# Performance work log

Measured on AMD Instinct MI355X. Metric: run time of the kernel, lower is better.

Reference implementation:

```python
import jax, jax.numpy as jnp
import numpy as np

B, N, D_MODEL, HEADS, DFF, M = 4, 4096, 1024, 16, 4096, 256
DH = D_MODEL // HEADS  # 64
EPS_K = 1e-4
LN_EPS = 1e-5


def setup_inputs() -> dict:
    key = jax.random.key(0)
    ks = jax.random.split(key, 12)
    s = 0.02
    return {
        "video": jax.random.normal(ks[0], (B, N, D_MODEL), jnp.float32),
        "Wq": jax.random.normal(ks[1], (D_MODEL, D_MODEL), jnp.float32) * s,
        "bq": jnp.zeros((D_MODEL,), jnp.float32),
        "Wk": jax.random.normal(ks[2], (D_MODEL, D_MODEL), jnp.float32) * s,
        "bk": jnp.zeros((D_MODEL,), jnp.float32),
        "Wv": jax.random.normal(ks[3], (D_MODEL, D_MODEL), jnp.float32) * s,
        "bv": jnp.zeros((D_MODEL,), jnp.float32),
        "Wo": jax.random.normal(ks[4], (D_MODEL, D_MODEL), jnp.float32) * s,
        "bo": jnp.zeros((D_MODEL,), jnp.float32),
        "proj": jax.random.normal(ks[5], (M, DH), jnp.float32),  # random-feature matrix (buffer)
        "W1": jax.random.normal(ks[6], (DFF, D_MODEL), jnp.float32) * s,
        "b1": jnp.zeros((DFF,), jnp.float32),
        "W2": jax.random.normal(ks[7], (D_MODEL, DFF), jnp.float32) * s,
        "b2": jnp.zeros((D_MODEL,), jnp.float32),
        "g2": jnp.ones((D_MODEL,), jnp.float32),
        "be2": jnp.zeros((D_MODEL,), jnp.float32),
        "g3": jnp.ones((D_MODEL,), jnp.float32),
        "be3": jnp.zeros((D_MODEL,), jnp.float32),
    }


def softmax_kernel(x, proj, is_query):
    # FAVOR+ positive softmax random features (Performer).
    # x: [b,h,n,dh], proj: [m,dh]
    norm = x.shape[-1] ** -0.25  # data normalizer 1/d^{1/4}
    ratio = proj.shape[0] ** -0.5
    xp = jnp.einsum("bhnd,md->bhnm", x * norm, proj)
    diag = jnp.sum(jnp.square(x), axis=-1, keepdims=True) * 0.5 * (norm * norm)
    if is_query:
        stab = jnp.max(xp, axis=-1, keepdims=True)
    else:
        stab = jnp.max(xp, axis=(-1, -2), keepdims=True)
    return ratio * (jnp.exp(xp - diag - stab) + EPS_K)


def layer_norm(x, g, b):
    mu = jnp.mean(x, axis=-1, keepdims=True)
    var = jnp.mean(jnp.square(x - mu), axis=-1, keepdims=True)
    return (x - mu) * jax.lax.rsqrt(var + LN_EPS) * g + b


def reference(video, Wq, bq, Wk, bk, Wv, bv, Wo, bo, proj,
              W1, b1, W2, b2, g2, be2, g3, be3):
    b, n, d = video.shape
    split = lambda t: t.reshape(b, n, HEADS, DH).transpose(0, 2, 1, 3)  # [b,h,n,dh]
    q = split(video @ Wq.T + bq)
    k = split(video @ Wk.T + bk)
    v = split(video @ Wv.T + bv)

    qp = softmax_kernel(q, proj, is_query=True)   # [b,h,n,m]
    kp = softmax_kernel(k, proj, is_query=False)  # [b,h,n,m]

    # Non-causal linear attention: O(n*m*dh) instead of O(n^2)
    k_sum = jnp.sum(kp, axis=2)                              # [b,h,m]
    denom = jnp.einsum("bhnm,bhm->bhn", qp, k_sum)           # [b,h,n]
    ctx = jnp.einsum("bhnm,bhnd->bhmd", kp, v)               # [b,h,m,dh]
    out = jnp.einsum("bhnm,bhmd->bhnd", qp, ctx) / denom[..., None]

    attn = out.transpose(0, 2, 1, 3).reshape(b, n, d) @ Wo.T + bo
    x = layer_norm(video + attn, g2, be2)  # dropout is identity in eval
    ff = jax.nn.relu(x @ W1.T + b1) @ W2.T + b2
    return layer_norm(x + ff, g3, be3)
```

## Files before the change

kernel.cpp:

```cpp
#include <hip/hip_runtime.h>
#include <hip/hip_bf16.h>

#define N_TOK   4096
#define DMODEL  1024
#define NHEADS  16
#define DH      64
#define MFEAT   256
#define DFF     4096
#define BATCH   4
#define ROWS    (BATCH * N_TOK)

#define NORMF      0.35355339059327373f
#define HALF_NORM2 0.0625f
#define RATIO      0.0625f
#define EPSK       1e-4f
#define LNEPS      1e-5f

typedef unsigned short ushort_t;
using bfrag = __attribute__((ext_vector_type(8))) short;
using facc  = __attribute__((ext_vector_type(4))) float;
using ush8  = __attribute__((ext_vector_type(8))) unsigned short;

__device__ __forceinline__ float b2f(ushort_t u) {
    return __bfloat162float(__builtin_bit_cast(__hip_bfloat16, u));
}
__device__ __forceinline__ ushort_t f2b(float f) {
    return __builtin_bit_cast(ushort_t, __float2bfloat16(f));
}
__device__ __forceinline__ void stC(float* p, float v) { *p = v; }
__device__ __forceinline__ void stC(ushort_t* p, float v) { *p = f2b(v); }

__device__ __forceinline__ void gload_lds16(const void* g, void* l) {
    __builtin_amdgcn_global_load_lds(
        (const __attribute__((address_space(1))) unsigned int*)g,
        (__attribute__((address_space(3))) unsigned int*)l, 16, 0, 0);
}

__device__ __forceinline__ unsigned fkey(float f) {
    unsigned u = __float_as_uint(f);
    return (u & 0x80000000u) ? ~u : (u | 0x80000000u);
}
__device__ __forceinline__ float fdec(unsigned k) {
    return (k & 0x80000000u) ? __uint_as_float(k ^ 0x80000000u) : __uint_as_float(~k);
}

__global__ __launch_bounds__(256) void cvt_bf16(const float* __restrict__ s,
                                                ushort_t* __restrict__ d, int n4) {
    int i = blockIdx.x * 256 + threadIdx.x;
    if (i >= n4) return;
    float4 v = ((const float4*)s)[i];
    ((ushort4*)d)[i] = make_ushort4(f2b(v.x), f2b(v.y), f2b(v.z), f2b(v.w));
}

template <int FJ, typename OT>
__global__ __launch_bounds__(256) void gemm_mfma(
    const ushort_t* __restrict__ A, const ushort_t* __restrict__ W,
    const float* __restrict__ bias, OT* __restrict__ C,
    int Nout, int K, int relu)
{
    constexpr int BN = FJ * 32;
    __shared__ short As[2][128 * 32];
    __shared__ short Ws[2][BN * 32];
    const int t = threadIdx.x;
    const unsigned nwg = gridDim.x * gridDim.y;
    const unsigned flat = blockIdx.y * gridDim.x + blockIdx.x;
    const unsigned cpx = nwg >> 3;
    const unsigned wg = (flat & 7) * cpx + (flat >> 3);
    const int m0 = (int)(wg / gridDim.x) * 128, n0 = (int)(wg % gridDim.x) * BN;
    const int lane = t & 63, wave = t >> 6;
    const int wr = (wave >> 1) * 64, wc = (wave & 1) * (FJ * 16);
    const int lm = lane & 15, kq = (lane >> 4) * 8;
    facc acc[4][FJ];
#pragma unroll
    for (int i = 0; i < 4; ++i)
#pragma unroll
        for (int j = 0; j < FJ; ++j) acc[i][j] = (facc){0.f, 0.f, 0.f, 0.f};

    auto stage = [&](int b, int k0) {
#pragma unroll
        for (int it = 0; it < 2; ++it) {
            int ch = t + it * 256;
            gload_lds16(A + (size_t)(m0 + (ch >> 2)) * K + k0 + (ch & 3) * 8, &As[b][ch * 8]);
        }
#pragma unroll
        for (int it = 0; it < BN / 64; ++it) {
            int ch = t + it * 256;
            gload_lds16(W + (size_t)(n0 + (ch >> 2)) * K + k0 + (ch & 3) * 8, &Ws[b][ch * 8]);
        }
    };

    stage(0, 0);
    __syncthreads();
    int buf = 0;
    for (int k0 = 0; k0 < K; k0 += 32) {
        if (k0 + 32 < K) stage(buf ^ 1, k0 + 32);
        bfrag af[4], bf[FJ];
#pragma unroll
        for (int i = 0; i < 4; ++i) af[i] = *(bfrag*)&As[buf][(wr + i * 16 + lm) * 32 + kq];
#pragma unroll
        for (int j = 0; j < FJ; ++j) bf[j] = *(bfrag*)&Ws[buf][(wc + j * 16 + lm) * 32 + kq];
#pragma unroll
        for (int i = 0; i < 4; ++i)
#pragma unroll
            for (int j = 0; j < FJ; ++j)
                acc[i][j] = __builtin_amdgcn_mfma_f32_16x16x32_bf16(af[i], bf[j], acc[i][j], 0, 0, 0);
        __syncthreads();
        buf ^= 1;
    }
    const int rq = (lane >> 4) * 4;
#pragma unroll
    for (int i = 0; i < 4; ++i)
#pragma unroll
        for (int j = 0; j < FJ; ++j) {
            int col = n0 + wc + j * 16 + lm;
            float bc = bias[col];
#pragma unroll
            for (int r = 0; r < 4; ++r) {
                int row = m0 + wr + i * 16 + rq + r;
                float v = acc[i][j][r] + bc;
                if (relu) v = fmaxf(v, 0.f);
                stC(C + (size_t)row * Nout + col, v);
            }
        }
}

__global__ __launch_bounds__(256) void gemm_kv(
    const ushort_t* __restrict__ A,
    const ushort_t* __restrict__ WK, const ushort_t* __restrict__ WV,
    const float* __restrict__ bK, const float* __restrict__ bV,
    ushort_t* __restrict__ CK, ushort_t* __restrict__ CV)
{
    __shared__ short As[2][128 * 32];
    __shared__ short Ws[2][128 * 32];
    const int t = threadIdx.x;
    const unsigned nwg = gridDim.x * gridDim.y;
    const unsigned flat = blockIdx.y * gridDim.x + blockIdx.x;
    const unsigned cpx = nwg >> 3;
    const unsigned wg = (flat & 7) * cpx + (flat >> 3);
    const int m0 = (int)(wg / gridDim.x) * 128;
    const int nt = (int)(wg % gridDim.x);
    const ushort_t* W = (nt < 8) ? WK : WV;
    const float* bias = (nt < 8) ? bK : bV;
    ushort_t* C = (nt < 8) ? CK : CV;
    const int n0 = (nt & 7) * 128;
    const int lane = t & 63, wave = t >> 6;
    const int wr = (wave >> 1) * 64, wc = (wave & 1) * 64;
    const int lm = lane & 15, kq = (lane >> 4) * 8;
    facc acc[4][4];
#pragma unroll
    for (int i = 0; i < 4; ++i)
#pragma unroll
        for (int j = 0; j < 4; ++j) acc[i][j] = (facc){0.f, 0.f, 0.f, 0.f};

    auto stage = [&](int b, int k0) {
#pragma unroll
        for (int it = 0; it < 2; ++it) {
            int ch = t + it * 256;
            gload_lds16(A + (size_t)(m0 + (ch >> 2)) * DMODEL + k0 + (ch & 3) * 8, &As[b][ch * 8]);
            gload_lds16(W + (size_t)(n0 + (ch >> 2)) * DMODEL + k0 + (ch & 3) * 8, &Ws[b][ch * 8]);
        }
    };

    stage(0, 0);
    __syncthreads();
    int buf = 0;
    for (int k0 = 0; k0 < DMODEL; k0 += 32) {
        if (k0 + 32 < DMODEL) stage(buf ^ 1, k0 + 32);
        bfrag af[4], bf[4];
#pragma unroll
        for (int i = 0; i < 4; ++i) af[i] = *(bfrag*)&As[buf][(wr + i * 16 + lm) * 32 + kq];
#pragma unroll
        for (int j = 0; j < 4; ++j) bf[j] = *(bfrag*)&Ws[buf][(wc + j * 16 + lm) * 32 + kq];
#pragma unroll
        for (int i = 0; i < 4; ++i)
#pragma unroll
            for (int j = 0; j < 4; ++j)
                acc[i][j] = __builtin_amdgcn_mfma_f32_16x16x32_bf16(af[i], bf[j], acc[i][j], 0, 0, 0);
        __syncthreads();
        buf ^= 1;
    }
    const int rq = (lane >> 4) * 4;
#pragma unroll
    for (int i = 0; i < 4; ++i)
#pragma unroll
        for (int j = 0; j < 4; ++j) {
            int col = n0 + wc + j * 16 + lm;
            float bc = bias[col];
#pragma unroll
            for (int r = 0; r < 4; ++r) {
                int row = m0 + wr + i * 16 + rq + r;
                C[(size_t)row * DMODEL + col] = f2b(acc[i][j][r] + bc);
            }
        }
}

__global__ __launch_bounds__(256) void vt_kernel(
    const ushort_t* __restrict__ V, ushort_t* __restrict__ VT)
{
    __shared__ ushort_t tile[64][68];
    const int t = threadIdx.x;
    const int n0 = blockIdx.x * 64, h = blockIdx.y;
#pragma unroll
    for (int i = 0; i < 4; ++i) {
        int idx = t + i * 256;
        int nl = idx >> 4, d4 = (idx & 15) * 4;
        ushort4 v = *(const ushort4*)(V + (size_t)(n0 + nl) * DMODEL + h * DH + d4);
        tile[nl][d4 + 0] = v.x; tile[nl][d4 + 1] = v.y;
        tile[nl][d4 + 2] = v.z; tile[nl][d4 + 3] = v.w;
    }
    __syncthreads();
#pragma unroll
    for (int i = 0; i < 4; ++i) {
        int idx = t + i * 256;
        int d = idx >> 4, n4 = (idx & 15) * 4;
        ushort4 o = make_ushort4(tile[n4][d], tile[n4 + 1][d], tile[n4 + 2][d], tile[n4 + 3][d]);
        *(ushort4*)(VT + (size_t)h * DH * N_TOK + (size_t)d * N_TOK + n0 + n4) = o;
    }
}

__global__ __launch_bounds__(256) void diagk_kernel(
    const ushort_t* __restrict__ Kb, float* __restrict__ diagK)
{
    const int lane = threadIdx.x & 63, wave = threadIdx.x >> 6;
    const int n = blockIdx.x * 4 + wave;
    const ushort_t* kr = Kb + (size_t)n * DMODEL + lane * 16;
    ush8 a = *(const ush8*)kr;
    ush8 b = *(const ush8*)(kr + 8);
    float s = 0.f;
#pragma unroll
    for (int e = 0; e < 8; ++e) { float x = b2f(a[e]); s += x * x; }
#pragma unroll
    for (int e = 0; e < 8; ++e) { float x = b2f(b[e]); s += x * x; }
    s += __shfl_xor(s, 1);
    s += __shfl_xor(s, 2);
    if ((lane & 3) == 0) diagK[(size_t)(lane >> 2) * N_TOK + n] = s;
}

__global__ __launch_bounds__(256) void xk_kernel(
    const ushort_t* __restrict__ projBF,
    const ushort_t* __restrict__ Kb,
    const float* __restrict__ diagK,
    unsigned* __restrict__ kmax16,
    ushort_t* __restrict__ KP,
    int mode)
{
    __shared__ short As[2][128 * 32];
    __shared__ short Ws[2][128 * 32];
    const int t = threadIdx.x;
    const int m0 = blockIdx.x * 128, n0 = blockIdx.y * 128, h = blockIdx.z;
    const ushort_t* Kh = Kb + h * DH;
    const int lane = t & 63, wave = t >> 6;
    const int wr = (wave >> 1) * 64, wc = (wave & 1) * 64;
    const int lm = lane & 15, kq = (lane >> 4) * 8;
    facc acc[4][4];
#pragma unroll
    for (int i = 0; i < 4; ++i)
#pragma unroll
        for (int j = 0; j < 4; ++j) acc[i][j] = (facc){0.f, 0.f, 0.f, 0.f};

    auto stage = [&](int b, int k0) {
#pragma unroll
        for (int it = 0; it < 2; ++it) {
            int ch = t + it * 256;
            gload_lds16(projBF + (size_t)(m0 + (ch >> 2)) * DH + k0 + (ch & 3) * 8, &As[b][ch * 8]);
            gload_lds16(Kh + (size_t)(n0 + (ch >> 2)) * DMODEL + k0 + (ch & 3) * 8, &Ws[b][ch * 8]);
        }
    };

    stage(0, 0);
    __syncthreads();
    int buf = 0;
    for (int k0 = 0; k0 < DH; k0 += 32) {
        if (k0 + 32 < DH) stage(buf ^ 1, k0 + 32);
        bfrag af[4], bf[4];
#pragma unroll
        for (int i = 0; i < 4; ++i) af[i] = *(bfrag*)&As[buf][(wr + i * 16 + lm) * 32 + kq];
#pragma unroll
        for (int j = 0; j < 4; ++j) bf[j] = *(bfrag*)&Ws[buf][(wc + j * 16 + lm) * 32 + kq];
#pragma unroll
        for (int i = 0; i < 4; ++i)
#pragma unroll
            for (int j = 0; j < 4; ++j)
                acc[i][j] = __builtin_amdgcn_mfma_f32_16x16x32_bf16(af[i], bf[j], acc[i][j], 0, 0, 0);
        __syncthreads();
        buf ^= 1;
    }
    const int rq = (lane >> 4) * 4;
    if (mode == 0) {
        float mx = -1e30f;
#pragma unroll
        for (int i = 0; i < 4; ++i)
#pragma unroll
            for (int j = 0; j < 4; ++j)
#pragma unroll
                for (int r = 0; r < 4; ++r) mx = fmaxf(mx, acc[i][j][r]);
        mx *= NORMF;
#pragma unroll
        for (int o = 32; o >= 1; o >>= 1) mx = fmaxf(mx, __shfl_xor(mx, o));
        if (lane == 0) atomicMax(kmax16 + h, fkey(mx));
    } else {
        const float stab = fdec(kmax16[h]);
        ushort_t* kb = KP + (size_t)h * MFEAT * N_TOK;
#pragma unroll
        for (int j = 0; j < 4; ++j) {
            int n = n0 + wc + j * 16 + lm;
            float dg = HALF_NORM2 * diagK[(size_t)h * N_TOK + n] + stab;
#pragma unroll
            for (int i = 0; i < 4; ++i)
#pragma unroll
                for (int r = 0; r < 4; ++r) {
                    int m = m0 + wr + i * 16 + rq + r;
                    float x = NORMF * acc[i][j][r];
                    kb[(size_t)m * N_TOK + n] = f2b(RATIO * (expf(x - dg) + EPSK));
                }
        }
    }
}

__global__ __launch_bounds__(256) void ksum_kernel(
    const ushort_t* __restrict__ KP, float* __restrict__ ksum)
{
    const int lane = threadIdx.x & 63, wave = threadIdx.x >> 6;
    const int row = blockIdx.x * 4 + wave;
    const ushort_t* kr = KP + (size_t)row * N_TOK;
    float s = 0.f;
#pragma unroll
    for (int it = 0; it < 8; ++it) {
        ush8 v = *(const ush8*)(kr + it * 512 + lane * 8);
#pragma unroll
        for (int e = 0; e < 8; ++e) s += b2f(v[e]);
    }
#pragma unroll
    for (int o = 32; o >= 1; o >>= 1) s += __shfl_xor(s, o);
    if (lane == 0) ksum[row] = s;
}

__global__ __launch_bounds__(256) void ctx_mfma(
    const ushort_t* __restrict__ KP, const ushort_t* __restrict__ VT,
    float* __restrict__ ctxp)
{
    __shared__ short As[2][128 * 32];
    __shared__ short Vs[2][64 * 32];
    const int t = threadIdx.x;
    const int z = blockIdx.x, mh = blockIdx.y, h = blockIdx.z;
    const ushort_t* A = KP + (size_t)h * MFEAT * N_TOK + (size_t)mh * 128 * N_TOK;
    const ushort_t* W = VT + (size_t)h * DH * N_TOK;
    const int lane = t & 63, wave = t >> 6;
    const int wr = (wave >> 1) * 64, wc = (wave & 1) * 32;
    const int lm = lane & 15, kq = (lane >> 4) * 8;
    facc acc[4][2];
#pragma unroll
    for (int i = 0; i < 4; ++i)
#pragma unroll
        for (int j = 0; j < 2; ++j) acc[i][j] = (facc){0.f, 0.f, 0.f, 0.f};

    auto stage = [&](int b, int k0) {
#pragma unroll
        for (int it = 0; it < 2; ++it) {
            int ch = t + it * 256;
            gload_lds16(A + (size_t)(ch >> 2) * N_TOK + k0 + (ch & 3) * 8, &As[b][ch * 8]);
        }
        gload_lds16(W + (size_t)(t >> 2) * N_TOK + k0 + (t & 3) * 8, &Vs[b][t * 8]);
    };

    const int kbeg = z * 512, kend = kbeg + 512;
    stage(0, kbeg);
    __syncthreads();
    int buf = 0;
    for (int k0 = kbeg; k0 < kend; k0 += 32) {
        if (k0 + 32 < kend) stage(buf ^ 1, k0 + 32);
        bfrag af[4], bf[2];
#pragma unroll
        for (int i = 0; i < 4; ++i) af[i] = *(bfrag*)&As[buf][(wr + i * 16 + lm) * 32 + kq];
#pragma unroll
        for (int j = 0; j < 2; ++j) bf[j] = *(bfrag*)&Vs[buf][(wc + j * 16 + lm) * 32 + kq];
#pragma unroll
        for (int i = 0; i < 4; ++i)
#pragma unroll
            for (int j = 0; j < 2; ++j)
                acc[i][j] = __builtin_amdgcn_mfma_f32_16x16x32_bf16(af[i], bf[j], acc[i][j], 0, 0, 0);
        __syncthreads();
        buf ^= 1;
    }
    const int rq = (lane >> 4) * 4;
    float* cb = ctxp + ((size_t)(z * NHEADS + h) * MFEAT + mh * 128) * DH;
#pragma unroll
    for (int i = 0; i < 4; ++i)
#pragma unroll
        for (int j = 0; j < 2; ++j)
#pragma unroll
            for (int r = 0; r < 4; ++r) {
                int m = wr + i * 16 + rq + r;
                int d = wc + j * 16 + lm;
                cb[(size_t)m * DH + d] = acc[i][j][r];
            }
}

__global__ __launch_bounds__(256) void ctx_transpose(
    const float* __restrict__ ctxp, ushort_t* __restrict__ ctxT)
{
    __shared__ float tile[64][65];
    const int h = blockIdx.x >> 2, mb = blockIdx.x & 3, t = threadIdx.x;
#pragma unroll
    for (int i = 0; i < 16; ++i) {
        int idx = t + i * 256;
        int ml = idx >> 6, d = idx & 63;
        int m = mb * 64 + ml;
        float s = 0.f;
#pragma unroll
        for (int z = 0; z < 8; ++z)
            s += ctxp[((size_t)(z * NHEADS + h) * MFEAT + m) * DH + d];
        tile[ml][d] = s;
    }
    __syncthreads();
    ushort_t* ob = ctxT + (size_t)h * DH * MFEAT;
#pragma unroll
    for (int i = 0; i < 16; ++i) {
        int idx = t + i * 256;
        int d = idx >> 6, ml = idx & 63;
        ob[(size_t)d * MFEAT + mb * 64 + ml] = f2b(tile[ml][d]);
    }
}

__global__ __launch_bounds__(256) void xp_gemm(
    const float* __restrict__ Q, const ushort_t* __restrict__ projBF,
    ushort_t* __restrict__ XP)
{
    __shared__ short As[128][40];
    __shared__ short Ws[128][40];
    const int t = threadIdx.x;
    const int m0 = blockIdx.x * 128, n0v = blockIdx.y * 128, h = blockIdx.z;
    const float* Qb = Q + h * DH;
    const int lane = t & 63, wave = t >> 6;
    const int wr = (wave >> 1) * 64, wc = (wave & 1) * 64;
    const int lm = lane & 15, kq = (lane >> 4) * 8;
    facc acc[4][4];
#pragma unroll
    for (int i = 0; i < 4; ++i)
#pragma unroll
        for (int j = 0; j < 4; ++j) acc[i][j] = (facc){0.f, 0.f, 0.f, 0.f};

    for (int k0 = 0; k0 < 64; k0 += 32) {
#pragma unroll
        for (int it = 0; it < 4; ++it) {
            int ch = t + it * 256;
            int row = ch >> 3, c4 = (ch & 7) * 4;
            float4 v = *(const float4*)(Qb + (size_t)(n0v + row) * DMODEL + k0 + c4);
            As[row][c4 + 0] = (short)f2b(v.x);
            As[row][c4 + 1] = (short)f2b(v.y);
            As[row][c4 + 2] = (short)f2b(v.z);
            As[row][c4 + 3] = (short)f2b(v.w);
        }
#pragma unroll
        for (int it = 0; it < 2; ++it) {
            int ch = t + it * 256;
            int row = ch >> 2, c8 = (ch & 3) * 8;
            *(uint4*)&Ws[row][c8] = *(const uint4*)(projBF + (size_t)(m0 + row) * DH + k0 + c8);
        }
        __syncthreads();
        bfrag af[4], bf[4];
#pragma unroll
        for (int i = 0; i < 4; ++i) af[i] = *(bfrag*)&As[wr + i * 16 + lm][kq];
#pragma unroll
        for (int j = 0; j < 4; ++j) bf[j] = *(bfrag*)&Ws[wc + j * 16 + lm][kq];
#pragma unroll
        for (int i = 0; i < 4; ++i)
#pragma unroll
            for (int j = 0; j < 4; ++j)
                acc[i][j] = __builtin_amdgcn_mfma_f32_16x16x32_bf16(af[i], bf[j], acc[i][j], 0, 0, 0);
        __syncthreads();
    }
    const int rq = (lane >> 4) * 4;
    ushort_t* xb = XP + (size_t)h * N_TOK * MFEAT;
#pragma unroll
    for (int i = 0; i < 4; ++i)
#pragma unroll
        for (int j = 0; j < 4; ++j) {
            int col = m0 + wc + j * 16 + lm;
#pragma unroll
            for (int r = 0; r < 4; ++r) {
                int row = n0v + wr + i * 16 + rq + r;
                xb[(size_t)row * MFEAT + col] = f2b(NORMF * acc[i][j][r]);
            }
        }
}

__global__ __launch_bounds__(256) void qp_kernel(
    ushort_t* __restrict__ XP, const float* __restrict__ Q,
    const float* __restrict__ ksum, float* __restrict__ denom)
{
    const int lane = threadIdx.x & 63, wave = threadIdx.x >> 6;
    const int row0 = (blockIdx.x * 4 + wave) * 8;
    for (int rr = 0; rr < 8; ++rr) {
        const int row = row0 + rr;
        const int h = row >> 12, n = row & 4095;
        ushort_t* xr = XP + (size_t)row * MFEAT + lane * 4;
        ushort4 xv = *(ushort4*)xr;
        float x0 = b2f(xv.x), x1 = b2f(xv.y), x2 = b2f(xv.z), x3 = b2f(xv.w);
        float qv = Q[(size_t)n * DMODEL + h * DH + lane];
        float ss = qv * qv;
#pragma unroll
        for (int o = 32; o >= 1; o >>= 1) ss += __shfl_xor(ss, o);
        float mx = fmaxf(fmaxf(x0, x1), fmaxf(x2, x3));
#pragma unroll
        for (int o = 32; o >= 1; o >>= 1) mx = fmaxf(mx, __shfl_xor(mx, o));
        const float sh = HALF_NORM2 * ss + mx;
        float p0 = RATIO * (expf(x0 - sh) + EPSK);
        float p1 = RATIO * (expf(x1 - sh) + EPSK);
        float p2 = RATIO * (expf(x2 - sh) + EPSK);
        float p3 = RATIO * (expf(x3 - sh) + EPSK);
        ushort4 pv = make_ushort4(f2b(p0), f2b(p1), f2b(p2), f2b(p3));
        *(ushort4*)xr = pv;
        float4 ks4 = *(const float4*)(ksum + h * MFEAT + lane * 4);
        float dn = b2f(pv.x) * ks4.x + b2f(pv.y) * ks4.y + b2f(pv.z) * ks4.z + b2f(pv.w) * ks4.w;
#pragma unroll
        for (int o = 32; o >= 1; o >>= 1) dn += __shfl_xor(dn, o);
        if (lane == 0) denom[row] = dn;
    }
}

__global__ __launch_bounds__(256) void out_gemm(
    const ushort_t* __restrict__ XP, const ushort_t* __restrict__ ctxT,
    const float* __restrict__ denom, ushort_t* __restrict__ OUT)
{
    __shared__ short As[2][128 * 32];
    __shared__ short Ws[2][64 * 32];
    const int t = threadIdx.x;
    const int n0 = blockIdx.x * 128, h = blockIdx.y;
    const ushort_t* A = XP + (size_t)h * N_TOK * MFEAT;
    const ushort_t* W = ctxT + (size_t)h * DH * MFEAT;
    const float* dnb = denom + (size_t)h * N_TOK;
    ushort_t* ob = OUT + h * DH;
    const int lane = t & 63, wave = t >> 6;
    const int wr = (wave >> 1) * 64, wc = (wave & 1) * 32;
    const int lm = lane & 15, kq = (lane >> 4) * 8;
    facc acc[4][2];
#pragma unroll
    for (int i = 0; i < 4; ++i)
#pragma unroll
        for (int j = 0; j < 2; ++j) acc[i][j] = (facc){0.f, 0.f, 0.f, 0.f};

    auto stage = [&](int b, int k0) {
#pragma unroll
        for (int it = 0; it < 2; ++it) {
            int ch = t + it * 256;
            gload_lds16(A + (size_t)(n0 + (ch >> 2)) * MFEAT + k0 + (ch & 3) * 8, &As[b][ch * 8]);
        }
        gload_lds16(W + (size_t)(t >> 2) * MFEAT + k0 + (t & 3) * 8, &Ws[b][t * 8]);
    };

    stage(0, 0);
    __syncthreads();
    int buf = 0;
    for (int k0 = 0; k0 < MFEAT; k0 += 32) {
        if (k0 + 32 < MFEAT) stage(buf ^ 1, k0 + 32);
        bfrag af[4], bf[2];
#pragma unroll
        for (int i = 0; i < 4; ++i) af[i] = *(bfrag*)&As[buf][(wr + i * 16 + lm) * 32 + kq];
#pragma unroll
        for (int j = 0; j < 2; ++j) bf[j] = *(bfrag*)&Ws[buf][(wc + j * 16 + lm) * 32 + kq];
#pragma unroll
        for (int i = 0; i < 4; ++i)
#pragma unroll
            for (int j = 0; j < 2; ++j)
                acc[i][j] = __builtin_amdgcn_mfma_f32_16x16x32_bf16(af[i], bf[j], acc[i][j], 0, 0, 0);
        __syncthreads();
        buf ^= 1;
    }
    const int rq = (lane >> 4) * 4;
#pragma unroll
    for (int i = 0; i < 4; ++i)
#pragma unroll
        for (int r = 0; r < 4; ++r) {
            int row = n0 + wr + i * 16 + rq + r;
            float inv = 1.f / dnb[row];
#pragma unroll
            for (int j = 0; j < 2; ++j) {
                int col = wc + j * 16 + lm;
                ob[(size_t)row * DMODEL + col] = f2b(acc[i][j][r] * inv);
            }
        }
}

__global__ __launch_bounds__(256) void ln_kernel(
    const float* __restrict__ A, const void* __restrict__ Badd, int badd_bf16,
    const float* __restrict__ g, const float* __restrict__ bb,
    float* __restrict__ out, ushort_t* __restrict__ out_bf)
{
    __shared__ float red[8];
    const int row = blockIdx.x, t = threadIdx.x;
    const int lane = t & 63, wave = t >> 6;
    float4 av = ((const float4*)(A + (size_t)row * DMODEL))[t];
    float a0, a1, a2, a3;
    if (badd_bf16) {
        ushort4 bv4 = ((const ushort4*)Badd)[(size_t)row * (DMODEL / 4) + t];
        a0 = b2f(bv4.x); a1 = b2f(bv4.y); a2 = b2f(bv4.z); a3 = b2f(bv4.w);
    } else {
        float4 bf4 = ((const float4*)Badd)[(size_t)row * (DMODEL / 4) + t];
        a0 = bf4.x; a1 = bf4.y; a2 = bf4.z; a3 = bf4.w;
    }
    float v0 = av.x + a0, v1 = av.y + a1, v2 = av.z + a2, v3 = av.w + a3;
    float s = v0 + v1 + v2 + v3;
#pragma unroll
    for (int o = 32; o >= 1; o >>= 1) s += __shfl_xor(s, o);
    if (lane == 0) red[wave] = s;
    __syncthreads();
    float mu = (red[0] + red[1] + red[2] + red[3]) * (1.f / DMODEL);
    float d0 = v0 - mu, d1 = v1 - mu, d2 = v2 - mu, d3 = v3 - mu;
    float sq = d0 * d0 + d1 * d1 + d2 * d2 + d3 * d3;
#pragma unroll
    for (int o = 32; o >= 1; o >>= 1) sq += __shfl_xor(sq, o);
    if (lane == 0) red[4 + wave] = sq;
    __syncthreads();
    float rstd = rsqrtf((red[4] + red[5] + red[6] + red[7]) * (1.f / DMODEL) + LNEPS);
    float4 gv = ((const float4*)g)[t];
    float4 bv = ((const float4*)bb)[t];
    float o0 = d0 * rstd * gv.x + bv.x;
    float o1 = d1 * rstd * gv.y + bv.y;
    float o2 = d2 * rstd * gv.z + bv.z;
    float o3 = d3 * rstd * gv.w + bv.w;
    ((float4*)(out + (size_t)row * DMODEL))[t] = make_float4(o0, o1, o2, o3);
    if (out_bf)
        ((ushort4*)(out_bf + (size_t)row * DMODEL))[t] =
            make_ushort4(f2b(o0), f2b(o1), f2b(o2), f2b(o3));
}

extern "C" void kernel_launch(void* const* d_in, const int* in_sizes, int n_in,
                              void* d_out, int out_size, void* d_ws, size_t ws_size,
                              hipStream_t stream)
{
    const float* video = (const float*)d_in[0];
    const float* Wq = (const float*)d_in[1];
    const float* bq = (const float*)d_in[2];
    const float* Wk = (const float*)d_in[3];
    const float* bk = (const float*)d_in[4];
    const float* Wv = (const float*)d_in[5];
    const float* bv = (const float*)d_in[6];
    const float* Wo = (const float*)d_in[7];
    const float* bo = (const float*)d_in[8];
    const float* proj = (const float*)d_in[9];
    const float* W1 = (const float*)d_in[10];
    const float* b1 = (const float*)d_in[11];
    const float* W2 = (const float*)d_in[12];
    const float* b2 = (const float*)d_in[13];
    const float* g2 = (const float*)d_in[14];
    const float* be2 = (const float*)d_in[15];
    const float* g3 = (const float*)d_in[16];
    const float* be3 = (const float*)d_in[17];

    char* ws = (char*)d_ws;
    const size_t MB = 1048576ull;
    ushort_t* videoBF = (ushort_t*)(ws + 0);
    ushort_t* Kb   = (ushort_t*)(ws + 32 * MB);
    ushort_t* XBFb = (ushort_t*)(ws + 32 * MB);
    ushort_t* Vb   = (ushort_t*)(ws + 40 * MB);
    ushort_t* Fb   = (ushort_t*)(ws + 40 * MB);
    ushort_t* VTb  = (ushort_t*)(ws + 48 * MB);
    ushort_t* Yb   = (ushort_t*)(ws + 48 * MB);
    ushort_t* KP   = (ushort_t*)(ws + 56 * MB);
    ushort_t* Hb   = (ushort_t*)(ws + 56 * MB);
    ushort_t* ctxTb = (ushort_t*)(ws + 93847552ull + MB);
    char* smalls = ws + 91 * MB + 393216ull;
    float*    diagK  = (float*)(smalls);
    float*    ksum   = (float*)(smalls + 262144);
    float*    denomB = (float*)(smalls + 278528);
    unsigned* kmax16 = (unsigned*)(smalls + 540672);
    ushort_t* projBF = (ushort_t*)(smalls + 541184);
    float*    ctxp  = (float*)(ws + 92 * MB);
    ushort_t* OUTb = (ushort_t*)(ws + 92 * MB);
    ushort_t* WqBF = (ushort_t*)(ws + 100 * MB);
    ushort_t* WkBF = (ushort_t*)(ws + 102 * MB);
    ushort_t* WvBF = (ushort_t*)(ws + 104 * MB);
    ushort_t* WoBF = (ushort_t*)(ws + 106 * MB);
    ushort_t* W1BF = (ushort_t*)(ws + 108 * MB);
    ushort_t* W2BF = (ushort_t*)(ws + 116 * MB);
    float* Qbuf = (float*)d_out;

    dim3 blk(256);

    cvt_bf16<<<dim3(ROWS * DMODEL / 1024), blk, 0, stream>>>(video, videoBF, ROWS * DMODEL / 4);
    cvt_bf16<<<dim3(DMODEL * DMODEL / 1024), blk, 0, stream>>>(Wq, WqBF, DMODEL * DMODEL / 4);
    cvt_bf16<<<dim3(DMODEL * DMODEL / 1024), blk, 0, stream>>>(Wk, WkBF, DMODEL * DMODEL / 4);
    cvt_bf16<<<dim3(DMODEL * DMODEL / 1024), blk, 0, stream>>>(Wv, WvBF, DMODEL * DMODEL / 4);
    cvt_bf16<<<dim3(DMODEL * DMODEL / 1024), blk, 0, stream>>>(Wo, WoBF, DMODEL * DMODEL / 4);
    cvt_bf16<<<dim3(DFF * DMODEL / 1024), blk, 0, stream>>>(W1, W1BF, DFF * DMODEL / 4);
    cvt_bf16<<<dim3(DFF * DMODEL / 1024), blk, 0, stream>>>(W2, W2BF, DFF * DMODEL / 4);
    cvt_bf16<<<dim3(16), blk, 0, stream>>>(proj, projBF, MFEAT * DH / 4);

    gemm_mfma<4, float><<<dim3(8, ROWS / 128), blk, 0, stream>>>(
        videoBF, WqBF, bq, Qbuf, DMODEL, DMODEL, 0);

    dim3 gP(8, 32);

    for (int b = 0; b < BATCH; ++b) {
        const size_t roff = (size_t)b * N_TOK;
        const ushort_t* vbf = videoBF + roff * DMODEL;
        float* Qb = Qbuf + roff * DMODEL;

        gemm_kv<<<dim3(16, 32), blk, 0, stream>>>(vbf, WkBF, WvBF, bk, bv, Kb, Vb);
        vt_kernel<<<dim3(64, 16), blk, 0, stream>>>(Vb, VTb);
        diagk_kernel<<<dim3(1024), blk, 0, stream>>>(Kb, diagK);

        hipMemsetAsync(kmax16, 0, 64, stream);

        xk_kernel<<<dim3(2, 32, 16), blk, 0, stream>>>(projBF, Kb, diagK, kmax16, KP, 0);
        xk_kernel<<<dim3(2, 32, 16), blk, 0, stream>>>(projBF, Kb, diagK, kmax16, KP, 1);
        ksum_kernel<<<dim3(1024), blk, 0, stream>>>(KP, ksum);
        ctx_mfma<<<dim3(8, 2, 16), blk, 0, stream>>>(KP, VTb, ctxp);
        ctx_transpose<<<dim3(64), blk, 0, stream>>>(ctxp, ctxTb);

        xp_gemm<<<dim3(2, 32, 16), blk, 0, stream>>>(Qb, projBF, KP);
        qp_kernel<<<dim3(2048), blk, 0, stream>>>(KP, Qb, ksum, denomB);
        out_gemm<<<dim3(32, 16), blk, 0, stream>>>(KP, ctxTb, denomB, OUTb);

        gemm_mfma<4, ushort_t><<<gP, blk, 0, stream>>>(OUTb, WoBF, bo, Yb, DMODEL, DMODEL, 0);
        ln_kernel<<<dim3(N_TOK), blk, 0, stream>>>(
            video + roff * DMODEL, Yb, 1, g2, be2, Qb, XBFb);
        gemm_mfma<4, ushort_t><<<dim3(32, 32), blk, 0, stream>>>(
            XBFb, W1BF, b1, Hb, DFF, DMODEL, 1);
        gemm_mfma<2, ushort_t><<<dim3(16, 32), blk, 0, stream>>>(
            Hb, W2BF, b2, Fb, DMODEL, DFF, 0);
        ln_kernel<<<dim3(N_TOK), blk, 0, stream>>>(
            Qb, Fb, 1, g3, be3, Qb, nullptr);
    }
}
```

Measured before the change: 1.658 ms.

## Batch KV and Wo GEMMs over batch pairs and split-K the W2 GEMM with atomics

Restructures the schedule so the K/V projection and the Wo projection run on two batches at once, giving larger grids per launch. The attention output is written into the V buffer to save workspace. The FFN second GEMM is split over K into two slices that accumulate with float atomics into a bias-seeded fp32 buffer. This raises occupancy for the tall-K GEMM at the cost of atomic traffic, an extra seeding kernel and an extra fp32-to-bf16 conversion pass. The workspace layout is reshuffled to fit the paired buffers, and xk_kernel's two-step K loop is unrolled with both stages issued up front.

```diff
diff --git a/kernel.cpp b/kernel.cpp
--- a/kernel.cpp
+++ b/kernel.cpp
@@ -52,7 +52,14 @@
     ((ushort4*)d)[i] = make_ushort4(f2b(v.x), f2b(v.y), f2b(v.z), f2b(v.w));
 }
 
-template <int FJ, typename OT>
+__global__ __launch_bounds__(256) void seed_bias(float* __restrict__ C,
+                                                 const float* __restrict__ bias) {
+    const int row = blockIdx.x, t = threadIdx.x;
+    float4 b4 = ((const float4*)bias)[t];
+    ((float4*)(C + (size_t)row * DMODEL))[t] = b4;
+}
+
+template <int FJ, typename OT, bool ATOMIC>
 __global__ __launch_bounds__(256) void gemm_mfma(
     const ushort_t* __restrict__ A, const ushort_t* __restrict__ W,
     const float* __restrict__ bias, OT* __restrict__ C,
@@ -67,6 +74,8 @@
     const unsigned cpx = nwg >> 3;
     const unsigned wg = (flat & 7) * cpx + (flat >> 3);
     const int m0 = (int)(wg / gridDim.x) * 128, n0 = (int)(wg % gridDim.x) * BN;
+    const int kslice = K / (int)gridDim.z;
+    const int kbeg = blockIdx.z * kslice, kend = kbeg + kslice;
     const int lane = t & 63, wave = t >> 6;
     const int wr = (wave >> 1) * 64, wc = (wave & 1) * (FJ * 16);
     const int lm = lane & 15, kq = (lane >> 4) * 8;
@@ -88,38 +97,46 @@
             gload_lds16(W + (size_t)(n0 + (ch >> 2)) * K + k0 + (ch & 3) * 8, &Ws[b][ch * 8]);
         }
     };
-
-    stage(0, 0);
-    __syncthreads();
-    int buf = 0;
-    for (int k0 = 0; k0 < K; k0 += 32) {
-        if (k0 + 32 < K) stage(buf ^ 1, k0 + 32);
+    auto compute = [&](int b) {
         bfrag af[4], bf[FJ];
 #pragma unroll
-        for (int i = 0; i < 4; ++i) af[i] = *(bfrag*)&As[buf][(wr + i * 16 + lm) * 32 + kq];
-#pragma unroll
-        for (int j = 0; j < FJ; ++j) bf[j] = *(bfrag*)&Ws[buf][(wc + j * 16 + lm) * 32 + kq];
+        for (int i = 0; i < 4; ++i) af[i] = *(bfrag*)&As[b][(wr + i * 16 + lm) * 32 + kq];
+#pragma unroll
+        for (int j = 0; j < FJ; ++j) bf[j] = *(bfrag*)&Ws[b][(wc + j * 16 + lm) * 32 + kq];
 #pragma unroll
         for (int i = 0; i < 4; ++i)
 #pragma unroll
             for (int j = 0; j < FJ; ++j)
                 acc[i][j] = __builtin_amdgcn_mfma_f32_16x16x32_bf16(af[i], bf[j], acc[i][j], 0, 0, 0);
+    };
+
+    stage(0, kbeg);
+    __syncthreads();
+    int buf = 0;
+    for (int k0 = kbeg; k0 < kend; k0 += 32) {
+        if (k0 + 32 < kend) stage(buf ^ 1, k0 + 32);
+        compute(buf);
         __syncthreads();
         buf ^= 1;
     }
+
     const int rq = (lane >> 4) * 4;
 #pragma unroll
     for (int i = 0; i < 4; ++i)
 #pragma unroll
         for (int j = 0; j < FJ; ++j) {
             int col = n0 + wc + j * 16 + lm;
-            float bc = bias[col];
+            float bc = ATOMIC ? 0.f : bias[col];
 #pragma unroll
             for (int r = 0; r < 4; ++r) {
                 int row = m0 + wr + i * 16 + rq + r;
-                float v = acc[i][j][r] + bc;
-                if (relu) v = fmaxf(v, 0.f);
-                stC(C + (size_t)row * Nout + col, v);
+                if constexpr (ATOMIC) {
+                    atomicAdd((float*)C + (size_t)row * Nout + col, acc[i][j][r]);
+                } else {
+                    float v = acc[i][j][r] + bc;
+                    if (relu) v = fmaxf(v, 0.f);
+                    stC(C + (size_t)row * Nout + col, v);
+                }
             }
         }
 }
@@ -160,25 +177,29 @@
             gload_lds16(W + (size_t)(n0 + (ch >> 2)) * DMODEL + k0 + (ch & 3) * 8, &Ws[b][ch * 8]);
         }
     };
+    auto compute = [&](int b) {
+        bfrag af[4], bf[4];
+#pragma unroll
+        for (int i = 0; i < 4; ++i) af[i] = *(bfrag*)&As[b][(wr + i * 16 + lm) * 32 + kq];
+#pragma unroll
+        for (int j = 0; j < 4; ++j) bf[j] = *(bfrag*)&Ws[b][(wc + j * 16 + lm) * 32 + kq];
+#pragma unroll
+        for (int i = 0; i < 4; ++i)
+#pragma unroll
+            for (int j = 0; j < 4; ++j)
+                acc[i][j] = __builtin_amdgcn_mfma_f32_16x16x32_bf16(af[i], bf[j], acc[i][j], 0, 0, 0);
+    };
 
     stage(0, 0);
     __syncthreads();
     int buf = 0;
     for (int k0 = 0; k0 < DMODEL; k0 += 32) {
         if (k0 + 32 < DMODEL) stage(buf ^ 1, k0 + 32);
-        bfrag af[4], bf[4];
-#pragma unroll
-        for (int i = 0; i < 4; ++i) af[i] = *(bfrag*)&As[buf][(wr + i * 16 + lm) * 32 + kq];
-#pragma unroll
-        for (int j = 0; j < 4; ++j) bf[j] = *(bfrag*)&Ws[buf][(wc + j * 16 + lm) * 32 + kq];
-#pragma unroll
-        for (int i = 0; i < 4; ++i)
-#pragma unroll
-            for (int j = 0; j < 4; ++j)
-                acc[i][j] = __builtin_amdgcn_mfma_f32_16x16x32_bf16(af[i], bf[j], acc[i][j], 0, 0, 0);
+        compute(buf);
         __syncthreads();
         buf ^= 1;
     }
+
     const int rq = (lane >> 4) * 4;
 #pragma unroll
     for (int i = 0; i < 4; ++i)
@@ -266,25 +287,25 @@
             gload_lds16(Kh + (size_t)(n0 + (ch >> 2)) * DMODEL + k0 + (ch & 3) * 8, &Ws[b][ch * 8]);
         }
     };
-
-    stage(0, 0);
-    __syncthreads();
-    int buf = 0;
-    for (int k0 = 0; k0 < DH; k0 += 32) {
-        if (k0 + 32 < DH) stage(buf ^ 1, k0 + 32);
+    auto compute = [&](int b) {
         bfrag af[4], bf[4];
 #pragma unroll
-        for (int i = 0; i < 4; ++i) af[i] = *(bfrag*)&As[buf][(wr + i * 16 + lm) * 32 + kq];
-#pragma unroll
-        for (int j = 0; j < 4; ++j) bf[j] = *(bfrag*)&Ws[buf][(wc + j * 16 + lm) * 32 + kq];
+        for (int i = 0; i < 4; ++i) af[i] = *(bfrag*)&As[b][(wr + i * 16 + lm) * 32 + kq];
+#pragma unroll
+        for (int j = 0; j < 4; ++j) bf[j] = *(bfrag*)&Ws[b][(wc + j * 16 + lm) * 32 + kq];
 #pragma unroll
         for (int i = 0; i < 4; ++i)
 #pragma unroll
             for (int j = 0; j < 4; ++j)
                 acc[i][j] = __builtin_amdgcn_mfma_f32_16x16x32_bf16(af[i], bf[j], acc[i][j], 0, 0, 0);
-        __syncthreads();
-        buf ^= 1;
-    }
+    };
+
+    stage(0, 0);
+    stage(1, 32);
+    __syncthreads();
+    compute(0);
+    compute(1);
+
     const int rq = (lane >> 4) * 4;
     if (mode == 0) {
         float mx = -1e30f;
@@ -362,6 +383,18 @@
         }
         gload_lds16(W + (size_t)(t >> 2) * N_TOK + k0 + (t & 3) * 8, &Vs[b][t * 8]);
     };
+    auto compute = [&](int b) {
+        bfrag af[4], bf[2];
+#pragma unroll
+        for (int i = 0; i < 4; ++i) af[i] = *(bfrag*)&As[b][(wr + i * 16 + lm) * 32 + kq];
+#pragma unroll
+        for (int j = 0; j < 2; ++j) bf[j] = *(bfrag*)&Vs[b][(wc + j * 16 + lm) * 32 + kq];
+#pragma unroll
+        for (int i = 0; i < 4; ++i)
+#pragma unroll
+            for (int j = 0; j < 2; ++j)
+                acc[i][j] = __builtin_amdgcn_mfma_f32_16x16x32_bf16(af[i], bf[j], acc[i][j], 0, 0, 0);
+    };
 
     const int kbeg = z * 512, kend = kbeg + 512;
     stage(0, kbeg);
@@ -369,19 +402,11 @@
     int buf = 0;
     for (int k0 = kbeg; k0 < kend; k0 += 32) {
         if (k0 + 32 < kend) stage(buf ^ 1, k0 + 32);
-        bfrag af[4], bf[2];
-#pragma unroll
-        for (int i = 0; i < 4; ++i) af[i] = *(bfrag*)&As[buf][(wr + i * 16 + lm) * 32 + kq];
-#pragma unroll
-        for (int j = 0; j < 2; ++j) bf[j] = *(bfrag*)&Vs[buf][(wc + j * 16 + lm) * 32 + kq];
-#pragma unroll
-        for (int i = 0; i < 4; ++i)
-#pragma unroll
-            for (int j = 0; j < 2; ++j)
-                acc[i][j] = __builtin_amdgcn_mfma_f32_16x16x32_bf16(af[i], bf[j], acc[i][j], 0, 0, 0);
+        compute(buf);
         __syncthreads();
         buf ^= 1;
     }
+
     const int rq = (lane >> 4) * 4;
     float* cb = ctxp + ((size_t)(z * NHEADS + h) * MFEAT + mh * 128) * DH;
 #pragma unroll
@@ -548,25 +573,29 @@
         }
         gload_lds16(W + (size_t)(t >> 2) * MFEAT + k0 + (t & 3) * 8, &Ws[b][t * 8]);
     };
+    auto compute = [&](int b) {
+        bfrag af[4], bf[2];
+#pragma unroll
+        for (int i = 0; i < 4; ++i) af[i] = *(bfrag*)&As[b][(wr + i * 16 + lm) * 32 + kq];
+#pragma unroll
+        for (int j = 0; j < 2; ++j) bf[j] = *(bfrag*)&Ws[b][(wc + j * 16 + lm) * 32 + kq];
+#pragma unroll
+        for (int i = 0; i < 4; ++i)
+#pragma unroll
+            for (int j = 0; j < 2; ++j)
+                acc[i][j] = __builtin_amdgcn_mfma_f32_16x16x32_bf16(af[i], bf[j], acc[i][j], 0, 0, 0);
+    };
 
     stage(0, 0);
     __syncthreads();
     int buf = 0;
     for (int k0 = 0; k0 < MFEAT; k0 += 32) {
         if (k0 + 32 < MFEAT) stage(buf ^ 1, k0 + 32);
-        bfrag af[4], bf[2];
-#pragma unroll
-        for (int i = 0; i < 4; ++i) af[i] = *(bfrag*)&As[buf][(wr + i * 16 + lm) * 32 + kq];
-#pragma unroll
-        for (int j = 0; j < 2; ++j) bf[j] = *(bfrag*)&Ws[buf][(wc + j * 16 + lm) * 32 + kq];
-#pragma unroll
-        for (int i = 0; i < 4; ++i)
-#pragma unroll
-            for (int j = 0; j < 2; ++j)
-                acc[i][j] = __builtin_amdgcn_mfma_f32_16x16x32_bf16(af[i], bf[j], acc[i][j], 0, 0, 0);
+        compute(buf);
         __syncthreads();
         buf ^= 1;
     }
+
     const int rq = (lane >> 4) * 4;
 #pragma unroll
     for (int i = 0; i < 4; ++i)
@@ -651,29 +680,28 @@
     char* ws = (char*)d_ws;
     const size_t MB = 1048576ull;
     ushort_t* videoBF = (ushort_t*)(ws + 0);
-    ushort_t* Kb   = (ushort_t*)(ws + 32 * MB);
-    ushort_t* XBFb = (ushort_t*)(ws + 32 * MB);
-    ushort_t* Vb   = (ushort_t*)(ws + 40 * MB);
-    ushort_t* Fb   = (ushort_t*)(ws + 40 * MB);
-    ushort_t* VTb  = (ushort_t*)(ws + 48 * MB);
-    ushort_t* Yb   = (ushort_t*)(ws + 48 * MB);
-    ushort_t* KP   = (ushort_t*)(ws + 56 * MB);
-    ushort_t* Hb   = (ushort_t*)(ws + 56 * MB);
-    ushort_t* ctxTb = (ushort_t*)(ws + 93847552ull + MB);
-    char* smalls = ws + 91 * MB + 393216ull;
+    ushort_t* Kpair = (ushort_t*)(ws + 32 * MB);
+    ushort_t* Ypair = (ushort_t*)(ws + 32 * MB);
+    float*    Facc  = (float*)(ws + 32 * MB);
+    ushort_t* Vpair = (ushort_t*)(ws + 48 * MB);
+    ushort_t* XBF   = (ushort_t*)(ws + 48 * MB);
+    ushort_t* VTb   = (ushort_t*)(ws + 64 * MB);
+    ushort_t* W1BF  = (ushort_t*)(ws + 64 * MB);
+    ushort_t* KP    = (ushort_t*)(ws + 72 * MB);
+    ushort_t* Hb    = (ushort_t*)(ws + 72 * MB);
+    float*    ctxp  = (float*)(ws + 104 * MB);
+    ushort_t* W2BF  = (ushort_t*)(ws + 104 * MB);
+    ushort_t* ctxTb = (ushort_t*)(ws + 112 * MB);
+    char* smalls = ws + 112 * MB + 524288ull;
     float*    diagK  = (float*)(smalls);
     float*    ksum   = (float*)(smalls + 262144);
     float*    denomB = (float*)(smalls + 278528);
     unsigned* kmax16 = (unsigned*)(smalls + 540672);
     ushort_t* projBF = (ushort_t*)(smalls + 541184);
-    float*    ctxp  = (float*)(ws + 92 * MB);
-    ushort_t* OUTb = (ushort_t*)(ws + 92 * MB);
-    ushort_t* WqBF = (ushort_t*)(ws + 100 * MB);
-    ushort_t* WkBF = (ushort_t*)(ws + 102 * MB);
-    ushort_t* WvBF = (ushort_t*)(ws + 104 * MB);
-    ushort_t* WoBF = (ushort_t*)(ws + 106 * MB);
-    ushort_t* W1BF = (ushort_t*)(ws + 108 * MB);
-    ushort_t* W2BF = (ushort_t*)(ws + 116 * MB);
+    ushort_t* WqBF = (ushort_t*)(ws + 114 * MB);
+    ushort_t* WkBF = (ushort_t*)(ws + 116 * MB);
+    ushort_t* WvBF = (ushort_t*)(ws + 118 * MB);
+    ushort_t* WoBF = (ushort_t*)(ws + 120 * MB);
     float* Qbuf = (float*)d_out;
 
     dim3 blk(256);
@@ -683,44 +711,54 @@
     cvt_bf16<<<dim3(DMODEL * DMODEL / 1024), blk, 0, stream>>>(Wk, WkBF, DMODEL * DMODEL / 4);
     cvt_bf16<<<dim3(DMODEL * DMODEL / 1024), blk, 0, stream>>>(Wv, WvBF, DMODEL * DMODEL / 4);
     cvt_bf16<<<dim3(DMODEL * DMODEL / 1024), blk, 0, stream>>>(Wo, WoBF, DMODEL * DMODEL / 4);
+    cvt_bf16<<<dim3(16), blk, 0, stream>>>(proj, projBF, MFEAT * DH / 4);
+
+    gemm_mfma<4, float, false><<<dim3(8, 128, 1), blk, 0, stream>>>(
+        videoBF, WqBF, bq, Qbuf, DMODEL, DMODEL, 0);
+
+    for (int p = 0; p < 2; ++p) {
+        const ushort_t* vbfp = videoBF + (size_t)p * 8192 * DMODEL;
+
+        gemm_kv<<<dim3(16, 64), blk, 0, stream>>>(vbfp, WkBF, WvBF, bk, bv, Kpair, Vpair);
+
+        for (int bh = 0; bh < 2; ++bh) {
+            const int b = 2 * p + bh;
+            ushort_t* Kb = Kpair + (size_t)bh * N_TOK * DMODEL;
+            ushort_t* Vb = Vpair + (size_t)bh * N_TOK * DMODEL;
+            float* Qb = Qbuf + (size_t)b * N_TOK * DMODEL;
+
+            vt_kernel<<<dim3(64, 16), blk, 0, stream>>>(Vb, VTb);
+            diagk_kernel<<<dim3(1024), blk, 0, stream>>>(Kb, diagK);
+            hipMemsetAsync(kmax16, 0, 64, stream);
+            xk_kernel<<<dim3(2, 32, 16), blk, 0, stream>>>(projBF, Kb, diagK, kmax16, KP, 0);
+            xk_kernel<<<dim3(2, 32, 16), blk, 0, stream>>>(projBF, Kb, diagK, kmax16, KP, 1);
+            ksum_kernel<<<dim3(1024), blk, 0, stream>>>(KP, ksum);
+            ctx_mfma<<<dim3(8, 2, 16), blk, 0, stream>>>(KP, VTb, ctxp);
+            ctx_transpose<<<dim3(64), blk, 0, stream>>>(ctxp, ctxTb);
+            xp_gemm<<<dim3(2, 32, 16), blk, 0, stream>>>(Qb, projBF, KP);
+            qp_kernel<<<dim3(2048), blk, 0, stream>>>(KP, Qb, ksum, denomB);
+            out_gemm<<<dim3(32, 16), blk, 0, stream>>>(KP, ctxTb, denomB, Vb);
+        }
+
+        gemm_mfma<4, ushort_t, false><<<dim3(8, 64, 1), blk, 0, stream>>>(
+            Vpair, WoBF, bo, Ypair, DMODEL, DMODEL, 0);
+        ln_kernel<<<dim3(8192), blk, 0, stream>>>(
+            video + (size_t)p * 8192 * DMODEL, Ypair, 1, g2, be2,
+            Qbuf + (size_t)p * 8192 * DMODEL, nullptr);
+    }
+
     cvt_bf16<<<dim3(DFF * DMODEL / 1024), blk, 0, stream>>>(W1, W1BF, DFF * DMODEL / 4);
     cvt_bf16<<<dim3(DFF * DMODEL / 1024), blk, 0, stream>>>(W2, W2BF, DFF * DMODEL / 4);
-    cvt_bf16<<<dim3(16), blk, 0, stream>>>(proj, projBF, MFEAT * DH / 4);
-
-    gemm_mfma<4, float><<<dim3(8, ROWS / 128), blk, 0, stream>>>(
-        videoBF, WqBF, bq, Qbuf, DMODEL, DMODEL, 0);
-
-    dim3 gP(8, 32);
 
     for (int b = 0; b < BATCH; ++b) {
-        const size_t roff = (size_t)b * N_TOK;
-        const ushort_t* vbf = videoBF + roff * DMODEL;
-        float* Qb = Qbuf + roff * DMODEL;
-
-        gemm_kv<<<dim3(16, 32), blk, 0, stream>>>(vbf, WkBF, WvBF, bk, bv, Kb, Vb);
-        vt_kernel<<<dim3(64, 16), blk, 0, stream>>>(Vb, VTb);
-        diagk_kernel<<<dim3(1024), blk, 0, stream>>>(Kb, diagK);
-
-        hipMemsetAsync(kmax16, 0, 64, stream);
-
-        xk_kernel<<<dim3(2, 32, 16), blk, 0, stream>>>(projBF, Kb, diagK, kmax16, KP, 0);
-        xk_kernel<<<dim3(2, 32, 16), blk, 0, stream>>>(projBF, Kb, diagK, kmax16, KP, 1);
-        ksum_kernel<<<dim3(1024), blk, 0, stream>>>(KP, ksum);
-        ctx_mfma<<<dim3(8, 2, 16), blk, 0, stream>>>(KP, VTb, ctxp);
-        ctx_transpose<<<dim3(64), blk, 0, stream>>>(ctxp, ctxTb);
-
-        xp_gemm<<<dim3(2, 32, 16), blk, 0, stream>>>(Qb, projBF, KP);
-        qp_kernel<<<dim3(2048), blk, 0, stream>>>(KP, Qb, ksum, denomB);
-        out_gemm<<<dim3(32, 16), blk, 0, stream>>>(KP, ctxTb, denomB, OUTb);
-
-        gemm_mfma<4, ushort_t><<<gP, blk, 0, stream>>>(OUTb, WoBF, bo, Yb, DMODEL, DMODEL, 0);
+        float* Xb = Qbuf + (size_t)b * N_TOK * DMODEL;
+        cvt_bf16<<<dim3(4096), blk, 0, stream>>>(Xb, XBF, N_TOK * DMODEL / 4);
+        gemm_mfma<4, ushort_t, false><<<dim3(32, 32, 1), blk, 0, stream>>>(
+            XBF, W1BF, b1, Hb, DFF, DMODEL, 1);
+        seed_bias<<<dim3(N_TOK), blk, 0, stream>>>(Facc, b2);
+        gemm_mfma<2, float, true><<<dim3(16, 32, 2), blk, 0, stream>>>(
+            Hb, W2BF, nullptr, Facc, DMODEL, DFF, 0);
         ln_kernel<<<dim3(N_TOK), blk, 0, stream>>>(
-            video + roff * DMODEL, Yb, 1, g2, be2, Qb, XBFb);
-        gemm_mfma<4, ushort_t><<<dim3(32, 32), blk, 0, stream>>>(
-            XBFb, W1BF, b1, Hb, DFF, DMODEL, 1);
-        gemm_mfma<2, ushort_t><<<dim3(16, 32), blk, 0, stream>>>(
-            Hb, W2BF, b2, Fb, DMODEL, DFF, 0);
-        ln_kernel<<<dim3(N_TOK), blk, 0, stream>>>(
-            Qb, Fb, 1, g3, be3, Qb, nullptr);
-    }
-}
+            Xb, Facc, 0, g3, be3, Xb, nullptr);
+    }
+}
```

Result: no change. 1.664 ms (+0.3%).
